# Kernel tuning notes

Hardware: AMD Instinct MI355X
Metric: run time of the kernel (lower is better)

The kernel has to match this reference:

```python
import jax, jax.numpy as jnp
import numpy as np

N, E, F_IN, F_OUT, E_DIM = 8192, 65536, 256, 64, 32


def _xavier(k, shape, gain):
    fan_out, fan_in = shape
    bound = gain * jnp.sqrt(6.0 / (fan_in + fan_out))
    return jax.random.uniform(k, shape, jnp.float32, -bound, bound)


def setup_inputs() -> dict:
    key = jax.random.key(0)
    ks = jax.random.split(key, 10)
    gain = float(np.sqrt(2.0))  # calculate_gain('relu')
    return {
        "h_neigh": jax.random.normal(ks[0], (N, F_IN), jnp.float32),
        "h_self": jax.random.normal(ks[1], (N, F_IN), jnp.float32),
        "edge_features": jax.random.normal(ks[2], (E, E_DIM), jnp.float32),
        "W_preagg": _xavier(ks[3], (F_OUT, F_IN), gain),
        "W_self": _xavier(ks[4], (F_OUT, F_OUT), gain),
        "W_neigh": _xavier(ks[5], (F_OUT, F_OUT), gain),
        "W_edge": _xavier(ks[6], (F_OUT * F_OUT, E_DIM), gain),
        "b_edge": jnp.zeros((F_OUT * F_OUT,), jnp.float32),
        "src": jax.random.randint(ks[7], (E,), 0, N, jnp.int32),
        "dst": jax.random.randint(ks[8], (E,), 0, N, jnp.int32),
    }


def reference(h_neigh, h_self, edge_features, W_preagg, W_self, W_neigh, W_edge, b_edge, src, dst):
    relu = jax.nn.relu
    # fc_preagg (Linear no-bias + ReLU); dropout p=0 -> identity (eval mode)
    hn = relu(h_neigh @ W_preagg.T)   # [N, F_OUT]
    hs = relu(h_self @ W_preagg.T)    # [N, F_OUT]
    # edge_fc: Linear(edge_dim, F*F) + ReLU, viewed as [E, F, F]
    ew = relu(edge_features @ W_edge.T + b_edge).reshape(E, F_OUT, F_OUT)
    # DGL u_mul_e broadcast: m[e,i,j] = hn[src[e], j] * ew[e,i,j]
    # then mean over in-edges per dst node, then sum over dim i.
    # mean/sum commute with the i-sum, so fold i first: s[e,j] = sum_i ew[e,i,j]
    s = ew.sum(axis=1)                # [E, F_OUT]
    msg = hn[src] * s                 # [E, F_OUT]
    agg = jax.ops.segment_sum(msg, dst, num_segments=N)                      # [N, F_OUT]
    deg = jax.ops.segment_sum(jnp.ones((E,), jnp.float32), dst, num_segments=N)
    neigh = agg / jnp.maximum(deg, 1.0)[:, None]  # mean (0 for isolated nodes, as DGL)
    # fc_self / fc_neigh each include a ReLU, plus the outer ReLU
    z = relu(relu(hs @ W_self.T) + relu(neigh @ W_neigh.T))
    return z
```

## Files before the change

### kernel.cpp

```cpp
#include <hip/hip_runtime.h>
#include <hip/hip_bf16.h>

typedef __attribute__((ext_vector_type(8))) _Float16 f16x8;
typedef __attribute__((ext_vector_type(4))) float f32x4;

#define NNODES 8192
#define NEDGES 65536
#define FIN 256
#define FOUT 64
#define EDIM 32

#define WS_HN    0x000000u
#define WS_HS    0x200000u
#define WS_MSG   0x400000u
#define WS_DEG   0x1400000u
#define WS_OFF   0x1408000u
#define WS_RANK  0x1410000u
#define WS_PERM  0x1450000u
#define WS_GSRC  0x1490000u
#define WS_WEH   0x14D0000u
#define WS_WPREH 0x1510000u
#define WS_WFH   0x1518000u
#define WS_BF    0x1519000u
#define WS_WST   0x1520000u
#define WS_WNT   0x1524000u

__device__ __forceinline__ f16x8 pack8h(float4 v0, float4 v1) {
    f16x8 r;
    r[0] = (_Float16)v0.x; r[1] = (_Float16)v0.y;
    r[2] = (_Float16)v0.z; r[3] = (_Float16)v0.w;
    r[4] = (_Float16)v1.x; r[5] = (_Float16)v1.y;
    r[6] = (_Float16)v1.z; r[7] = (_Float16)v1.w;
    return r;
}

__global__ __launch_bounds__(256) void prep_count_kernel(
    const float* __restrict__ W_edge,
    const float* __restrict__ W_preagg,
    const float* __restrict__ W_self,
    const float* __restrict__ W_neigh,
    const float* __restrict__ b_edge,
    const int* __restrict__ dst,
    _Float16* __restrict__ weh,
    _Float16* __restrict__ wpreh,
    _Float16* __restrict__ wfh,
    float* __restrict__ bfold,
    float* __restrict__ wsT,
    float* __restrict__ wnT,
    int* __restrict__ deg,
    int* __restrict__ rank) {
    int b = blockIdx.x, t = threadIdx.x;
    if (b < 512) {
        int i = b * 256 + t;
        if (i < FOUT * FOUT * EDIM)
            weh[i] = (_Float16)W_edge[i];
        if (i < FOUT * FIN)
            wpreh[i] = (_Float16)W_preagg[i];
        if (i < FOUT * FOUT) {
            int o = i >> 6, k = i & 63;
            wsT[k * FOUT + o] = W_self[i];
            wnT[k * FOUT + o] = W_neigh[i];
        }
    } else if (b < 768) {
        int e = (b - 512) * 256 + t;
        rank[e] = atomicAdd(deg + dst[e], 1);
    } else {
        int idx = (b - 768) * 256 + t;
        int j = idx >> 5, k = idx & 31;
        float s = 0.f;
        #pragma unroll 4
        for (int i = 0; i < 64; ++i)
            s += W_edge[(i * 64 + j) * 32 + k];
        wfh[j * 32 + k] = (_Float16)s;
        if (idx < 64) {
            float sb = 0.f;
            #pragma unroll 4
            for (int i = 0; i < 64; ++i) sb += b_edge[i * 64 + idx];
            bfold[idx] = sb;
        }
    }
}

__global__ __launch_bounds__(256) void preagg_scan_kernel(
    const float* __restrict__ h_neigh,
    const float* __restrict__ h_self,
    const _Float16* __restrict__ wpreh,
    const int* __restrict__ deg,
    float* __restrict__ hn,
    float* __restrict__ hs,
    int* __restrict__ off) {
    __shared__ int wsum[4];
    int b = blockIdx.x, t = threadIdx.x;
    if (b == 256) {
        int lane = t & 63, w = t >> 6;
        int base = t * 32;
        int loc[32];
        int s = 0;
        #pragma unroll
        for (int i = 0; i < 32; ++i) { loc[i] = s; s += deg[base + i]; }
        int v = s;
        #pragma unroll
        for (int d = 1; d < 64; d <<= 1) {
            int u = __shfl_up(v, d);
            if (lane >= d) v += u;
        }
        if (lane == 63) wsum[w] = v;
        int threadExcl = v - s;
        __syncthreads();
        int wexcl = 0;
        for (int i = 0; i < w; ++i) wexcl += wsum[i];
        int tbase = wexcl + threadExcl;
        #pragma unroll
        for (int i = 0; i < 32; ++i) off[base + i] = tbase + loc[i];
        return;
    }
    int w = t >> 6, lane = t & 63;
    int rowm = lane & 15, kc = lane >> 4;
    int g0 = (b * 4 + w) * 16;
    const float* hsrc;
    float* outp;
    int r0;
    if (g0 < NNODES) { hsrc = h_neigh; outp = hn; r0 = g0; }
    else             { hsrc = h_self;  outp = hs; r0 = g0 - NNODES; }
    const float* arow = hsrc + (size_t)(r0 + rowm) * FIN;

    f32x4 acc[4];
    #pragma unroll
    for (int ot = 0; ot < 4; ++ot) acc[ot] = f32x4{0.f, 0.f, 0.f, 0.f};

    #pragma unroll 2
    for (int ks = 0; ks < 8; ++ks) {
        const float* p = arow + ks * 32 + kc * 8;
        float4 v0 = reinterpret_cast<const float4*>(p)[0];
        float4 v1 = reinterpret_cast<const float4*>(p)[1];
        f16x8 af = pack8h(v0, v1);
        #pragma unroll
        for (int ot = 0; ot < 4; ++ot) {
            f16x8 bh = *reinterpret_cast<const f16x8*>(
                wpreh + ((ot * 16 + rowm) * FIN + ks * 32 + kc * 8));
            acc[ot] = __builtin_amdgcn_mfma_f32_16x16x32_f16(af, bh, acc[ot], 0, 0, 0);
        }
    }
    #pragma unroll
    for (int ot = 0; ot < 4; ++ot)
        #pragma unroll
        for (int r = 0; r < 4; ++r)
            outp[(size_t)(r0 + kc * 4 + r) * FOUT + ot * 16 + rowm] =
                fmaxf(acc[ot][r], 0.f);
}

__global__ void fill_kernel(const int* __restrict__ src,
                            const int* __restrict__ dst,
                            const int* __restrict__ off,
                            const int* __restrict__ rank,
                            int* __restrict__ perm,
                            int* __restrict__ gsrc) {
    int e = blockIdx.x * 256 + threadIdx.x;
    int slot = off[dst[e]] + rank[e];
    perm[slot] = e;
    gsrc[slot] = src[e];
}

__global__ __launch_bounds__(256) void edge_kernel(
    const float* __restrict__ ef,
    const _Float16* __restrict__ weh,
    const float* __restrict__ b_edge,
    const _Float16* __restrict__ wfh,
    const float* __restrict__ bfold,
    const float* __restrict__ hn,
    const int* __restrict__ perm,
    const int* __restrict__ gsrc,
    float* __restrict__ msg) {
    int t = threadIdx.x;
    int cw = t >> 6, lane = t & 63;
    int rowm = lane & 15, kc = lane >> 4, k0 = kc * 8;
    int e0 = blockIdx.x * 64;
    int colbase = cw * 16 + rowm;

    f16x8 a[4];
    #pragma unroll
    for (int tt = 0; tt < 4; ++tt) {
        int eidx = perm[e0 + tt * 16 + rowm];
        const float* p = ef + (size_t)eidx * EDIM + k0;
        float4 v0 = reinterpret_cast<const float4*>(p)[0];
        float4 v1 = reinterpret_cast<const float4*>(p)[1];
        a[tt] = pack8h(v0, v1);
    }

    f16x8 wf = *reinterpret_cast<const f16x8*>(wfh + colbase * 32 + kc * 8);
    float bf = bfold[colbase];

    f32x4 sabs[4];
    #pragma unroll
    for (int tt = 0; tt < 4; ++tt) sabs[tt] = f32x4{0.f, 0.f, 0.f, 0.f};
    const f32x4 zc = {0.f, 0.f, 0.f, 0.f};

    unsigned wofs = (unsigned)colbase * 32 + (unsigned)kc * 8;
    unsigned bofs = (unsigned)colbase;

    #pragma unroll 4
    for (int g = 0; g < 64; ++g) {
        f16x8 bh = *reinterpret_cast<const f16x8*>(weh + wofs);
        float bias = b_edge[bofs];
        wofs += 2048;
        bofs += 64;
        #pragma unroll
        for (int tt = 0; tt < 4; ++tt) {
            f32x4 d = __builtin_amdgcn_mfma_f32_16x16x32_f16(a[tt], bh, zc, 0, 0, 0);
            sabs[tt][0] += __builtin_fabsf(d[0] + bias);
            sabs[tt][1] += __builtin_fabsf(d[1] + bias);
            sabs[tt][2] += __builtin_fabsf(d[2] + bias);
            sabs[tt][3] += __builtin_fabsf(d[3] + bias);
        }
    }

    #pragma unroll
    for (int tt = 0; tt < 4; ++tt) {
        f32x4 cin = {bf, bf, bf, bf};
        f32x4 d2 = __builtin_amdgcn_mfma_f32_16x16x32_f16(a[tt], wf, cin, 0, 0, 0);
        #pragma unroll
        for (int r = 0; r < 4; ++r) {
            int slot = e0 + tt * 16 + kc * 4 + r;
            int se = gsrc[slot];
            float hv = 0.5f * hn[(size_t)se * FOUT + colbase];
            msg[(size_t)slot * FOUT + colbase] = (d2[r] + sabs[tt][r]) * hv;
        }
    }
}

__global__ __launch_bounds__(256) void final_kernel(
    const float* __restrict__ hs,
    const float* __restrict__ msg,
    const int* __restrict__ deg,
    const int* __restrict__ off,
    const float* __restrict__ wsT,
    const float* __restrict__ wnT,
    float* __restrict__ out) {
    __shared__ float sm[4][2][FOUT];
    int t = threadIdx.x, w = t >> 6, lane = t & 63;
    int n = blockIdx.x * 4 + w;
    int o0 = off[n], d = deg[n];
    const float* mp = msg + (size_t)o0 * FOUT + lane;
    float acc = 0.f;
    int i = 0;
    for (; i + 4 <= d; i += 4) {
        float m0 = mp[(size_t)(i + 0) * FOUT];
        float m1 = mp[(size_t)(i + 1) * FOUT];
        float m2 = mp[(size_t)(i + 2) * FOUT];
        float m3 = mp[(size_t)(i + 3) * FOUT];
        acc += (m0 + m1) + (m2 + m3);
    }
    for (; i < d; ++i) acc += mp[(size_t)i * FOUT];
    float neigh = acc / fmaxf((float)d, 1.f);
    sm[w][0][lane] = neigh;
    sm[w][1][lane] = hs[(size_t)n * FOUT + lane];
    __syncthreads();
    float a1 = 0.f, a2 = 0.f;
    #pragma unroll 8
    for (int k = 0; k < FOUT; ++k) {
        a1 = fmaf(sm[w][1][k], wsT[k * FOUT + lane], a1);
        a2 = fmaf(sm[w][0][k], wnT[k * FOUT + lane], a2);
    }
    out[(size_t)n * FOUT + lane] = fmaxf(fmaxf(a1, 0.f) + fmaxf(a2, 0.f), 0.f);
}

extern "C" void kernel_launch(void* const* d_in, const int* in_sizes, int n_in,
                              void* d_out, int out_size, void* d_ws, size_t ws_size,
                              hipStream_t stream) {
    const float* h_neigh  = (const float*)d_in[0];
    const float* h_self   = (const float*)d_in[1];
    const float* ef       = (const float*)d_in[2];
    const float* W_preagg = (const float*)d_in[3];
    const float* W_self   = (const float*)d_in[4];
    const float* W_neigh  = (const float*)d_in[5];
    const float* W_edge   = (const float*)d_in[6];
    const float* b_edge   = (const float*)d_in[7];
    const int*   src      = (const int*)d_in[8];
    const int*   dst      = (const int*)d_in[9];
    float* out = (float*)d_out;
    char* ws = (char*)d_ws;

    float* hn    = (float*)(ws + WS_HN);
    float* hs    = (float*)(ws + WS_HS);
    float* msg   = (float*)(ws + WS_MSG);
    int*   deg   = (int*)(ws + WS_DEG);
    int*   off   = (int*)(ws + WS_OFF);
    int*   rank  = (int*)(ws + WS_RANK);
    int*   perm  = (int*)(ws + WS_PERM);
    int*   gsrc  = (int*)(ws + WS_GSRC);
    _Float16* weh   = (_Float16*)(ws + WS_WEH);
    _Float16* wpreh = (_Float16*)(ws + WS_WPREH);
    _Float16* wfh   = (_Float16*)(ws + WS_WFH);
    float* bfold = (float*)(ws + WS_BF);
    float* wsT   = (float*)(ws + WS_WST);
    float* wnT   = (float*)(ws + WS_WNT);

    hipMemsetAsync(ws + WS_DEG, 0, 0x8000, stream);

    prep_count_kernel<<<776, 256, 0, stream>>>(W_edge, W_preagg, W_self, W_neigh,
                                               b_edge, dst, weh, wpreh, wfh, bfold,
                                               wsT, wnT, deg, rank);
    preagg_scan_kernel<<<257, 256, 0, stream>>>(h_neigh, h_self, wpreh, deg,
                                                hn, hs, off);
    fill_kernel<<<NEDGES / 256, 256, 0, stream>>>(src, dst, off, rank, perm, gsrc);
    edge_kernel<<<1024, 256, 0, stream>>>(ef, weh, b_edge, wfh, bfold, hn,
                                          perm, gsrc, msg);
    final_kernel<<<NNODES / 4, 256, 0, stream>>>(hs, msg, deg, off, wsT, wnT, out);
}
```

Baseline: 88.48 us.

## Fuse fill into edge kernel and gather messages by perm in final kernel

The edge kernel now processes edges in original order, so edge features and src are read contiguously and messages are written in edge order. The permutation fill runs as extra blocks of the same launch, which removes one kernel launch and the gsrc array. The final kernel then gathers messages indirectly through perm, which trades the old sorted, coalesced reads for scattered 256-byte row reads. The edge bias is also folded into the MFMA accumulator input, saving one add per output element.

```diff
diff --git a/kernel.cpp b/kernel.cpp
--- a/kernel.cpp
+++ b/kernel.cpp
@@ -17,7 +17,6 @@
 #define WS_OFF   0x1408000u
 #define WS_RANK  0x1410000u
 #define WS_PERM  0x1450000u
-#define WS_GSRC  0x1490000u
 #define WS_WEH   0x14D0000u
 #define WS_WPREH 0x1510000u
 #define WS_WFH   0x1518000u
@@ -149,39 +148,34 @@
                 fmaxf(acc[ot][r], 0.f);
 }
 
-__global__ void fill_kernel(const int* __restrict__ src,
-                            const int* __restrict__ dst,
-                            const int* __restrict__ off,
-                            const int* __restrict__ rank,
-                            int* __restrict__ perm,
-                            int* __restrict__ gsrc) {
-    int e = blockIdx.x * 256 + threadIdx.x;
-    int slot = off[dst[e]] + rank[e];
-    perm[slot] = e;
-    gsrc[slot] = src[e];
-}
-
-__global__ __launch_bounds__(256) void edge_kernel(
+__global__ __launch_bounds__(256) void edge_fill_kernel(
     const float* __restrict__ ef,
     const _Float16* __restrict__ weh,
     const float* __restrict__ b_edge,
     const _Float16* __restrict__ wfh,
     const float* __restrict__ bfold,
     const float* __restrict__ hn,
-    const int* __restrict__ perm,
-    const int* __restrict__ gsrc,
-    float* __restrict__ msg) {
-    int t = threadIdx.x;
+    const int* __restrict__ src,
+    const int* __restrict__ dst,
+    const int* __restrict__ off,
+    const int* __restrict__ rank,
+    float* __restrict__ msg,
+    int* __restrict__ perm) {
+    int b = blockIdx.x, t = threadIdx.x;
+    if (b >= 1024) {
+        int e = (b - 1024) * 256 + t;
+        perm[off[dst[e]] + rank[e]] = e;
+        return;
+    }
     int cw = t >> 6, lane = t & 63;
     int rowm = lane & 15, kc = lane >> 4, k0 = kc * 8;
-    int e0 = blockIdx.x * 64;
+    int e0 = b * 64;
     int colbase = cw * 16 + rowm;
 
     f16x8 a[4];
     #pragma unroll
     for (int tt = 0; tt < 4; ++tt) {
-        int eidx = perm[e0 + tt * 16 + rowm];
-        const float* p = ef + (size_t)eidx * EDIM + k0;
+        const float* p = ef + (size_t)(e0 + tt * 16 + rowm) * EDIM + k0;
         float4 v0 = reinterpret_cast<const float4*>(p)[0];
         float4 v1 = reinterpret_cast<const float4*>(p)[1];
         a[tt] = pack8h(v0, v1);
@@ -193,7 +187,6 @@
     f32x4 sabs[4];
     #pragma unroll
     for (int tt = 0; tt < 4; ++tt) sabs[tt] = f32x4{0.f, 0.f, 0.f, 0.f};
-    const f32x4 zc = {0.f, 0.f, 0.f, 0.f};
 
     unsigned wofs = (unsigned)colbase * 32 + (unsigned)kc * 8;
     unsigned bofs = (unsigned)colbase;
@@ -204,26 +197,27 @@
         float bias = b_edge[bofs];
         wofs += 2048;
         bofs += 64;
+        f32x4 cin = {bias, bias, bias, bias};
         #pragma unroll
         for (int tt = 0; tt < 4; ++tt) {
-            f32x4 d = __builtin_amdgcn_mfma_f32_16x16x32_f16(a[tt], bh, zc, 0, 0, 0);
-            sabs[tt][0] += __builtin_fabsf(d[0] + bias);
-            sabs[tt][1] += __builtin_fabsf(d[1] + bias);
-            sabs[tt][2] += __builtin_fabsf(d[2] + bias);
-            sabs[tt][3] += __builtin_fabsf(d[3] + bias);
+            f32x4 d = __builtin_amdgcn_mfma_f32_16x16x32_f16(a[tt], bh, cin, 0, 0, 0);
+            sabs[tt][0] += __builtin_fabsf(d[0]);
+            sabs[tt][1] += __builtin_fabsf(d[1]);
+            sabs[tt][2] += __builtin_fabsf(d[2]);
+            sabs[tt][3] += __builtin_fabsf(d[3]);
         }
     }
 
     #pragma unroll
     for (int tt = 0; tt < 4; ++tt) {
-        f32x4 cin = {bf, bf, bf, bf};
-        f32x4 d2 = __builtin_amdgcn_mfma_f32_16x16x32_f16(a[tt], wf, cin, 0, 0, 0);
+        f32x4 cinf = {bf, bf, bf, bf};
+        f32x4 d2 = __builtin_amdgcn_mfma_f32_16x16x32_f16(a[tt], wf, cinf, 0, 0, 0);
         #pragma unroll
         for (int r = 0; r < 4; ++r) {
-            int slot = e0 + tt * 16 + kc * 4 + r;
-            int se = gsrc[slot];
+            int e = e0 + tt * 16 + kc * 4 + r;
+            int se = src[e];
             float hv = 0.5f * hn[(size_t)se * FOUT + colbase];
-            msg[(size_t)slot * FOUT + colbase] = (d2[r] + sabs[tt][r]) * hv;
+            msg[(size_t)e * FOUT + colbase] = (d2[r] + sabs[tt][r]) * hv;
         }
     }
 }
@@ -233,6 +227,7 @@
     const float* __restrict__ msg,
     const int* __restrict__ deg,
     const int* __restrict__ off,
+    const int* __restrict__ perm,
     const float* __restrict__ wsT,
     const float* __restrict__ wnT,
     float* __restrict__ out) {
@@ -240,17 +235,15 @@
     int t = threadIdx.x, w = t >> 6, lane = t & 63;
     int n = blockIdx.x * 4 + w;
     int o0 = off[n], d = deg[n];
-    const float* mp = msg + (size_t)o0 * FOUT + lane;
     float acc = 0.f;
     int i = 0;
-    for (; i + 4 <= d; i += 4) {
-        float m0 = mp[(size_t)(i + 0) * FOUT];
-        float m1 = mp[(size_t)(i + 1) * FOUT];
-        float m2 = mp[(size_t)(i + 2) * FOUT];
-        float m3 = mp[(size_t)(i + 3) * FOUT];
-        acc += (m0 + m1) + (m2 + m3);
-    }
-    for (; i < d; ++i) acc += mp[(size_t)i * FOUT];
+    for (; i + 2 <= d; i += 2) {
+        int ea = perm[o0 + i], eb = perm[o0 + i + 1];
+        float ma = msg[(size_t)ea * FOUT + lane];
+        float mb = msg[(size_t)eb * FOUT + lane];
+        acc += ma + mb;
+    }
+    if (i < d) acc += msg[(size_t)perm[o0 + i] * FOUT + lane];
     float neigh = acc / fmaxf((float)d, 1.f);
     sm[w][0][lane] = neigh;
     sm[w][1][lane] = hs[(size_t)n * FOUT + lane];
@@ -287,7 +280,6 @@
     int*   off   = (int*)(ws + WS_OFF);
     int*   rank  = (int*)(ws + WS_RANK);
     int*   perm  = (int*)(ws + WS_PERM);
-    int*   gsrc  = (int*)(ws + WS_GSRC);
     _Float16* weh   = (_Float16*)(ws + WS_WEH);
     _Float16* wpreh = (_Float16*)(ws + WS_WPREH);
     _Float16* wfh   = (_Float16*)(ws + WS_WFH);
@@ -302,8 +294,8 @@
                                                wsT, wnT, deg, rank);
     preagg_scan_kernel<<<257, 256, 0, stream>>>(h_neigh, h_self, wpreh, deg,
                                                 hn, hs, off);
-    fill_kernel<<<NEDGES / 256, 256, 0, stream>>>(src, dst, off, rank, perm, gsrc);
-    edge_kernel<<<1024, 256, 0, stream>>>(ef, weh, b_edge, wfh, bfold, hn,
-                                          perm, gsrc, msg);
-    final_kernel<<<NNODES / 4, 256, 0, stream>>>(hs, msg, deg, off, wsT, wnT, out);
-}
+    edge_fill_kernel<<<1280, 256, 0, stream>>>(ef, weh, b_edge, wfh, bfold, hn,
+                                               src, dst, off, rank, msg, perm);
+    final_kernel<<<NNODES / 4, 256, 0, stream>>>(hs, msg, deg, off, perm,
+                                                 wsT, wnT, out);
+}
```

Result: faster. 84.62 us (-4.4%).
